# Performance work log

Hardware: AMD Instinct MI355X
Metric: run time of the kernel (lower is better)

The kernel has to match this reference:

```python
import jax, jax.numpy as jnp
import numpy as np

TOP_K = 2
SCALING = 16.0 / 8.0  # alpha / rank


def setup_inputs() -> dict:
    key = jax.random.key(0)
    ks = jax.random.split(key, 9)
    B, V, D, P = 32, 21, 512, 64
    IN, OUT, E, R, H = D * P, 96, 8, 8, 256
    return {
        "x": jax.random.normal(ks[0], (B, V, D, P), jnp.float32),
        "W_base": jax.random.normal(ks[1], (OUT, IN), jnp.float32) * (IN ** -0.5),
        "b_base": jax.random.normal(ks[2], (OUT,), jnp.float32) * 0.01,
        "W1": jax.random.normal(ks[3], (H, D), jnp.float32) * (D ** -0.5),
        "b1": jax.random.normal(ks[4], (H,), jnp.float32) * 0.01,
        "W2": jax.random.normal(ks[5], (E, H), jnp.float32) * (H ** -0.5),
        "b2": jax.random.normal(ks[6], (E,), jnp.float32) * 0.01,
        "lora_A": jax.random.normal(ks[7], (E, R, IN), jnp.float32) * (IN ** -0.5),
        "lora_B": jax.random.normal(ks[8], (E, OUT, R), jnp.float32) * (R ** -0.5),
    }


def reference(x, W_base, b_base, W1, b1, W2, b2, lora_A, lora_B):
    B, V, D, P = x.shape
    E = lora_A.shape[0]
    # FlattenHead: flatten last two dims, then linear (dropout is identity in eval)
    flat = x.reshape(B, V, D * P)                      # [B, V, IN]
    base_out = flat @ W_base.T + b_base                # [B, V, OUT]
    # Router: pool over n_vars then patch dim -> [B, D]
    pooled = x.mean(axis=1).mean(axis=-1)
    h = jax.nn.relu(pooled @ W1.T + b1)
    logits = h @ W2.T + b2                             # [B, E]
    probs = jax.nn.softmax(logits, axis=-1)
    topw, topi = jax.lax.top_k(probs, TOP_K)           # [B, K]
    topw = topw / jnp.clip(topw.sum(-1, keepdims=True), 1e-6)
    # All LoRA experts (matches original dense compute), then weighted combine
    temp = jnp.einsum("bvi,eri->ebvr", flat, lora_A)   # [E, B, V, R]
    delta = jnp.einsum("ebvr,eor->ebvo", temp, lora_B) * SCALING  # [E, B, V, OUT]
    # Scatter top-k weights into dense [B, E] then combine (top-k sparse combine)
    w_full = jnp.zeros((B, E), x.dtype).at[jnp.arange(B)[:, None], topi].add(topw)
    moe_delta = jnp.einsum("be,ebvo->bvo", w_full, delta)
    return base_out + moe_delta, probs
```

## Files before the change

kernel.cpp:

```cpp
#include <hip/hip_runtime.h>

#define B_DIM 32
#define V_DIM 21
#define D_DIM 512
#define P_DIM 64
#define M_TOTAL 672
#define K_TOTAL 32768
#define OUT_DIM 96
#define E_DIM 8
#define R_DIM 8
#define H_DIM 256
#define N_TOTAL 160
#define SCALING 2.0f
#define POOL_SCALE (1.0f / (V_DIM * (float)P_DIM))

#define BM 64
#define BK 128
#define KSPLIT 64
#define K_PER_BLOCK (K_TOTAL / KSPLIT)
#define CHUNKS (K_PER_BLOCK / BK)
#define LDS_K (BK + 8)

typedef __attribute__((ext_vector_type(4))) float floatx4;
typedef __attribute__((ext_vector_type(8))) short short8;

__device__ __forceinline__ unsigned short f2bf(float f) {
  union { float f; unsigned int u; } v; v.f = f;
  unsigned int u = v.u + (0x7FFFu + ((v.u >> 16) & 1u));
  return (unsigned short)(u >> 16);
}

__global__ __launch_bounds__(256)
void convW_kernel(const float* __restrict__ W_base, const float* __restrict__ lora_A,
                  short* __restrict__ Wb) {
  size_t base = ((size_t)blockIdx.x * 256 + threadIdx.x) * 8;
  int row = (int)(base >> 15);
  int k = (int)(base & 32767);
  const float* src = (row < OUT_DIM) ? (W_base + ((size_t)row << 15) + k)
                                     : (lora_A + ((size_t)(row - OUT_DIM) << 15) + k);
  floatx4 v0 = ((const floatx4*)src)[0];
  floatx4 v1 = ((const floatx4*)src)[1];
  short8 sv;
  sv[0] = (short)f2bf(v0[0]); sv[1] = (short)f2bf(v0[1]);
  sv[2] = (short)f2bf(v0[2]); sv[3] = (short)f2bf(v0[3]);
  sv[4] = (short)f2bf(v1[0]); sv[5] = (short)f2bf(v1[1]);
  sv[6] = (short)f2bf(v1[2]); sv[7] = (short)f2bf(v1[3]);
  *(short8*)(Wb + base) = sv;
}

__global__ __launch_bounds__(256, 2)
void gemm_kernel(const float* __restrict__ x, const short* __restrict__ Wb,
                 float* __restrict__ S, float* __restrict__ pooled) {
  __shared__ short ldsA[BM * LDS_K];
  __shared__ short ldsW[N_TOTAL * LDS_K];
  __shared__ float lds_pool[5 * 8];
  const int tid = threadIdx.x;
  const int m0 = blockIdx.x * BM;
  const int kbase = blockIdx.y * K_PER_BLOCK;
  const int lane = tid & 63;
  const int wave = tid >> 6;
  const int quad = lane >> 4;
  const int l16 = lane & 15;
  const int mhalf = (wave & 1) * 32;
  const int nhalf = (wave >> 1) * 80;
  const int b_first = m0 / V_DIM;
  const int d_first = kbase >> 6;

  if (tid < 40) lds_pool[tid] = 0.0f;

  floatx4 acc[2][5];
  #pragma unroll
  for (int mt = 0; mt < 2; ++mt)
    #pragma unroll
    for (int nt = 0; nt < 5; ++nt) acc[mt][nt] = (floatx4)(0.0f);

  const int a_row0 = tid >> 4;
  const int a_g = tid & 15;

  floatx4 pa[8];
  short8  pw[10];

#define ISSUE_LOADS(c)                                                          \
  {                                                                             \
    const int kc = kbase + (c) * BK;                                            \
    _Pragma("unroll")                                                           \
    for (int it = 0; it < 4; ++it) {                                            \
      int row = a_row0 + it * 16;                                               \
      int m = m0 + row;                                                         \
      if (m < M_TOTAL) {                                                        \
        const floatx4* s4 = (const floatx4*)(x + (size_t)m * K_TOTAL + kc + a_g * 8); \
        pa[it * 2] = s4[0];                                                     \
        pa[it * 2 + 1] = s4[1];                                                 \
      } else {                                                                  \
        pa[it * 2] = (floatx4)(0.0f);                                           \
        pa[it * 2 + 1] = (floatx4)(0.0f);                                       \
      }                                                                         \
    }                                                                           \
    _Pragma("unroll")                                                           \
    for (int it = 0; it < 10; ++it) {                                           \
      int idx = it * 256 + tid;                                                 \
      int row = idx >> 4;                                                       \
      int g = idx & 15;                                                         \
      pw[it] = *(const short8*)(Wb + (size_t)row * K_TOTAL + kc + g * 8);       \
    }                                                                           \
  }

#define CONVERT_WRITE(c)                                                        \
  {                                                                             \
    const int kc = kbase + (c) * BK;                                            \
    _Pragma("unroll")                                                           \
    for (int it = 0; it < 4; ++it) {                                            \
      int row = a_row0 + it * 16;                                               \
      int m = m0 + row;                                                         \
      floatx4 v0 = pa[it * 2], v1 = pa[it * 2 + 1];                             \
      if (m < M_TOTAL) {                                                        \
        float sum8 = ((v0[0] + v0[1]) + (v0[2] + v0[3])) +                      \
                     ((v1[0] + v1[1]) + (v1[2] + v1[3]));                       \
        int b_local = (m / V_DIM) - b_first;                                    \
        int d_local = ((kc + a_g * 8) >> 6) - d_first;                          \
        atomicAdd(&lds_pool[b_local * 8 + d_local], sum8);                      \
      }                                                                         \
      short8 sv;                                                                \
      sv[0] = (short)f2bf(v0[0]); sv[1] = (short)f2bf(v0[1]);                   \
      sv[2] = (short)f2bf(v0[2]); sv[3] = (short)f2bf(v0[3]);                   \
      sv[4] = (short)f2bf(v1[0]); sv[5] = (short)f2bf(v1[1]);                   \
      sv[6] = (short)f2bf(v1[2]); sv[7] = (short)f2bf(v1[3]);                   \
      *(short8*)&ldsA[row * LDS_K + a_g * 8] = sv;                              \
    }                                                                           \
    _Pragma("unroll")                                                           \
    for (int it = 0; it < 10; ++it) {                                           \
      int idx = it * 256 + tid;                                                 \
      int row = idx >> 4;                                                       \
      int g = idx & 15;                                                         \
      *(short8*)&ldsW[row * LDS_K + g * 8] = pw[it];                            \
    }                                                                           \
  }

  ISSUE_LOADS(0);
  __syncthreads();
  CONVERT_WRITE(0);

  for (int c = 0; c < CHUNKS; ++c) {
    __syncthreads();
    if (c + 1 < CHUNKS) ISSUE_LOADS(c + 1);
    #pragma unroll
    for (int ks = 0; ks < 4; ++ks) {
      const int ko = ks * 32 + quad * 8;
      short8 a0 = *(const short8*)&ldsA[(mhalf + l16) * LDS_K + ko];
      short8 a1 = *(const short8*)&ldsA[(mhalf + 16 + l16) * LDS_K + ko];
      #pragma unroll
      for (int nt = 0; nt < 5; ++nt) {
        short8 b = *(const short8*)&ldsW[(nhalf + nt * 16 + l16) * LDS_K + ko];
        acc[0][nt] = __builtin_amdgcn_mfma_f32_16x16x32_bf16(a0, b, acc[0][nt], 0, 0, 0);
        acc[1][nt] = __builtin_amdgcn_mfma_f32_16x16x32_bf16(a1, b, acc[1][nt], 0, 0, 0);
      }
    }
    __syncthreads();
    if (c + 1 < CHUNKS) CONVERT_WRITE(c + 1);
  }

  #pragma unroll
  for (int mt = 0; mt < 2; ++mt)
    #pragma unroll
    for (int nt = 0; nt < 5; ++nt)
      #pragma unroll
      for (int r = 0; r < 4; ++r) {
        int m = m0 + mhalf + mt * 16 + quad * 4 + r;
        int n = nhalf + nt * 16 + l16;
        if (m < M_TOTAL) atomicAdd(&S[(size_t)m * N_TOTAL + n], acc[mt][nt][r]);
      }

  if (tid < 40) {
    int b = b_first + (tid >> 3);
    int d = d_first + (tid & 7);
    if (b < B_DIM)
      atomicAdd(&pooled[b * D_DIM + d], lds_pool[tid] * POOL_SCALE);
  }
}

__global__ __launch_bounds__(256)
void router_kernel(const float* __restrict__ pooled, const float* __restrict__ W1,
                   const float* __restrict__ b1, const float* __restrict__ W2,
                   const float* __restrict__ b2, float* __restrict__ wfull,
                   float* __restrict__ probs_out) {
  __shared__ float sp[D_DIM];
  __shared__ float sh[H_DIM];
  __shared__ float slog[E_DIM];
  const int b = blockIdx.x;
  const int t = threadIdx.x;
  sp[t] = pooled[b * D_DIM + t];
  sp[t + 256] = pooled[b * D_DIM + t + 256];
  __syncthreads();
  float acc = b1[t];
  const float* w1r = W1 + (size_t)t * D_DIM;
  for (int d = 0; d < D_DIM; ++d) acc += sp[d] * w1r[d];
  sh[t] = fmaxf(acc, 0.0f);
  __syncthreads();
  if (t < E_DIM) {
    float a = b2[t];
    const float* w2r = W2 + t * H_DIM;
    for (int j = 0; j < H_DIM; ++j) a += sh[j] * w2r[j];
    slog[t] = a;
  }
  __syncthreads();
  if (t == 0) {
    float p[E_DIM];
    float mx = slog[0];
    for (int e = 1; e < E_DIM; ++e) mx = fmaxf(mx, slog[e]);
    float se = 0.0f;
    for (int e = 0; e < E_DIM; ++e) { p[e] = __expf(slog[e] - mx); se += p[e]; }
    float inv = 1.0f / se;
    for (int e = 0; e < E_DIM; ++e) { p[e] *= inv; probs_out[b * E_DIM + e] = p[e]; }
    int i0 = 0;
    for (int e = 1; e < E_DIM; ++e) if (p[e] > p[i0]) i0 = e;
    int i1 = (i0 == 0) ? 1 : 0;
    for (int e = 0; e < E_DIM; ++e) if (e != i0 && p[e] > p[i1]) i1 = e;
    float s2 = p[i0] + p[i1];
    float invs = 1.0f / fmaxf(s2, 1e-6f);
    for (int e = 0; e < E_DIM; ++e) {
      float w = 0.0f;
      if (e == i0) w += p[i0] * invs;
      if (e == i1) w += p[i1] * invs;
      wfull[b * E_DIM + e] = w;
    }
  }
}

__global__ __launch_bounds__(256)
void combine_kernel(const float* __restrict__ S, const float* __restrict__ b_base,
                    const float* __restrict__ lora_B, const float* __restrict__ wfull,
                    float* __restrict__ out) {
  int idx = blockIdx.x * 256 + threadIdx.x;
  if (idx >= M_TOTAL * OUT_DIM) return;
  int bv = idx / OUT_DIM;
  int o = idx - bv * OUT_DIM;
  int b = bv / V_DIM;
  const float* srow = S + (size_t)bv * N_TOTAL;
  float base = srow[o] + b_base[o];
  float moe = 0.0f;
  #pragma unroll
  for (int e = 0; e < E_DIM; ++e) {
    float we = wfull[b * E_DIM + e];
    if (we != 0.0f) {
      const float* lb = lora_B + ((size_t)e * OUT_DIM + o) * R_DIM;
      const float* tr = srow + OUT_DIM + e * R_DIM;
      float d = 0.0f;
      #pragma unroll
      for (int r = 0; r < R_DIM; ++r) d += tr[r] * lb[r];
      moe += we * d;
    }
  }
  out[idx] = base + SCALING * moe;
}

extern "C" void kernel_launch(void* const* d_in, const int* in_sizes, int n_in,
                              void* d_out, int out_size, void* d_ws, size_t ws_size,
                              hipStream_t stream) {
  const float* x      = (const float*)d_in[0];
  const float* W_base = (const float*)d_in[1];
  const float* b_base = (const float*)d_in[2];
  const float* W1     = (const float*)d_in[3];
  const float* b1     = (const float*)d_in[4];
  const float* W2     = (const float*)d_in[5];
  const float* b2     = (const float*)d_in[6];
  const float* lora_A = (const float*)d_in[7];
  const float* lora_B = (const float*)d_in[8];
  float* out = (float*)d_out;

  float* ws     = (float*)d_ws;
  float* pooled = ws;
  float* S      = ws + 16384;
  float* wfull  = ws + 16384 + (size_t)M_TOTAL * N_TOTAL;
  short* Wb     = (short*)(wfull + 256);

  hipMemsetAsync(d_ws, 0, (16384 + (size_t)M_TOTAL * N_TOTAL) * sizeof(float), stream);

  convW_kernel<<<(N_TOTAL * K_TOTAL / 8 + 255) / 256, 256, 0, stream>>>(W_base, lora_A, Wb);
  gemm_kernel<<<dim3(11, KSPLIT), 256, 0, stream>>>(x, Wb, S, pooled);
  router_kernel<<<B_DIM, 256, 0, stream>>>(pooled, W1, b1, W2, b2, wfull,
                                           out + (size_t)M_TOTAL * OUT_DIM);
  combine_kernel<<<(M_TOTAL * OUT_DIM + 255) / 256, 256, 0, stream>>>(
      S, b_base, lora_B, wfull, out);
}
```

Measured before the change: 217.5 us.

## Load W fragments directly from global into registers, drop W LDS staging

The GEMM kernel no longer stages the bf16 weight tile in LDS. Each wave now reads its B-operand MFMA fragments straight from global memory, and only the activation tile goes through LDS. BK is halved to 64 and the pooling partial sums are reduced with a 16-lane shuffle before the LDS atomic. Smaller LDS use allows three blocks per CU instead of two, but the uncoalesced per-lane W loads are issued without prefetch, which can expose global latency and double the number of sync rounds.

```diff
diff --git a/kernel.cpp b/kernel.cpp
--- a/kernel.cpp
+++ b/kernel.cpp
@@ -15,7 +15,7 @@
 #define POOL_SCALE (1.0f / (V_DIM * (float)P_DIM))
 
 #define BM 64
-#define BK 128
+#define BK 64
 #define KSPLIT 64
 #define K_PER_BLOCK (K_TOTAL / KSPLIT)
 #define CHUNKS (K_PER_BLOCK / BK)
@@ -23,6 +23,7 @@
 
 typedef __attribute__((ext_vector_type(4))) float floatx4;
 typedef __attribute__((ext_vector_type(8))) short short8;
+typedef __attribute__((ext_vector_type(4))) short shortx4;
 
 __device__ __forceinline__ unsigned short f2bf(float f) {
   union { float f; unsigned int u; } v; v.f = f;
@@ -48,11 +49,10 @@
   *(short8*)(Wb + base) = sv;
 }
 
-__global__ __launch_bounds__(256, 2)
+__global__ __launch_bounds__(256, 3)
 void gemm_kernel(const float* __restrict__ x, const short* __restrict__ Wb,
                  float* __restrict__ S, float* __restrict__ pooled) {
   __shared__ short ldsA[BM * LDS_K];
-  __shared__ short ldsW[N_TOTAL * LDS_K];
   __shared__ float lds_pool[5 * 8];
   const int tid = threadIdx.x;
   const int m0 = blockIdx.x * BM;
@@ -74,85 +74,73 @@
     #pragma unroll
     for (int nt = 0; nt < 5; ++nt) acc[mt][nt] = (floatx4)(0.0f);
 
-  const int a_row0 = tid >> 4;
-  const int a_g = tid & 15;
-
-  floatx4 pa[8];
-  short8  pw[10];
-
-#define ISSUE_LOADS(c)                                                          \
+  floatx4 pa[4];
+
+#define ISSUE_A(c)                                                              \
   {                                                                             \
     const int kc = kbase + (c) * BK;                                            \
     _Pragma("unroll")                                                           \
     for (int it = 0; it < 4; ++it) {                                            \
-      int row = a_row0 + it * 16;                                               \
-      int m = m0 + row;                                                         \
-      if (m < M_TOTAL) {                                                        \
-        const floatx4* s4 = (const floatx4*)(x + (size_t)m * K_TOTAL + kc + a_g * 8); \
-        pa[it * 2] = s4[0];                                                     \
-        pa[it * 2 + 1] = s4[1];                                                 \
-      } else {                                                                  \
-        pa[it * 2] = (floatx4)(0.0f);                                           \
-        pa[it * 2 + 1] = (floatx4)(0.0f);                                       \
-      }                                                                         \
-    }                                                                           \
-    _Pragma("unroll")                                                           \
-    for (int it = 0; it < 10; ++it) {                                           \
       int idx = it * 256 + tid;                                                 \
       int row = idx >> 4;                                                       \
-      int g = idx & 15;                                                         \
-      pw[it] = *(const short8*)(Wb + (size_t)row * K_TOTAL + kc + g * 8);       \
+      int u = idx & 15;                                                         \
+      int m = m0 + row;                                                         \
+      pa[it] = (m < M_TOTAL)                                                    \
+          ? *(const floatx4*)(x + (size_t)m * K_TOTAL + kc + u * 4)             \
+          : (floatx4)(0.0f);                                                    \
     }                                                                           \
   }
 
 #define CONVERT_WRITE(c)                                                        \
   {                                                                             \
-    const int kc = kbase + (c) * BK;                                            \
     _Pragma("unroll")                                                           \
     for (int it = 0; it < 4; ++it) {                                            \
-      int row = a_row0 + it * 16;                                               \
-      int m = m0 + row;                                                         \
-      floatx4 v0 = pa[it * 2], v1 = pa[it * 2 + 1];                             \
-      if (m < M_TOTAL) {                                                        \
-        float sum8 = ((v0[0] + v0[1]) + (v0[2] + v0[3])) +                      \
-                     ((v1[0] + v1[1]) + (v1[2] + v1[3]));                       \
-        int b_local = (m / V_DIM) - b_first;                                    \
-        int d_local = ((kc + a_g * 8) >> 6) - d_first;                          \
-        atomicAdd(&lds_pool[b_local * 8 + d_local], sum8);                      \
-      }                                                                         \
-      short8 sv;                                                                \
-      sv[0] = (short)f2bf(v0[0]); sv[1] = (short)f2bf(v0[1]);                   \
-      sv[2] = (short)f2bf(v0[2]); sv[3] = (short)f2bf(v0[3]);                   \
-      sv[4] = (short)f2bf(v1[0]); sv[5] = (short)f2bf(v1[1]);                   \
-      sv[6] = (short)f2bf(v1[2]); sv[7] = (short)f2bf(v1[3]);                   \
-      *(short8*)&ldsA[row * LDS_K + a_g * 8] = sv;                              \
-    }                                                                           \
-    _Pragma("unroll")                                                           \
-    for (int it = 0; it < 10; ++it) {                                           \
       int idx = it * 256 + tid;                                                 \
       int row = idx >> 4;                                                       \
-      int g = idx & 15;                                                         \
-      *(short8*)&ldsW[row * LDS_K + g * 8] = pw[it];                            \
+      int u = idx & 15;                                                         \
+      int m = m0 + row;                                                         \
+      floatx4 v = pa[it];                                                       \
+       \
+      float s4 = (v[0] + v[1]) + (v[2] + v[3]);                                 \
+      s4 += __shfl_down(s4, 8, 16);                                             \
+      s4 += __shfl_down(s4, 4, 16);                                             \
+      s4 += __shfl_down(s4, 2, 16);                                             \
+      s4 += __shfl_down(s4, 1, 16);                                             \
+      if (u == 0 && m < M_TOTAL) {                                              \
+        int b_local = (m / V_DIM) - b_first;                                    \
+        atomicAdd(&lds_pool[b_local * 8 + (c)], s4);                            \
+      }                                                                         \
+      shortx4 sv;                                                               \
+      sv[0] = (short)f2bf(v[0]); sv[1] = (short)f2bf(v[1]);                     \
+      sv[2] = (short)f2bf(v[2]); sv[3] = (short)f2bf(v[3]);                     \
+      *(shortx4*)&ldsA[row * LDS_K + u * 4] = sv;                               \
     }                                                                           \
   }
 
-  ISSUE_LOADS(0);
+  ISSUE_A(0);
   __syncthreads();
   CONVERT_WRITE(0);
 
   for (int c = 0; c < CHUNKS; ++c) {
     __syncthreads();
-    if (c + 1 < CHUNKS) ISSUE_LOADS(c + 1);
-    #pragma unroll
-    for (int ks = 0; ks < 4; ++ks) {
+    if (c + 1 < CHUNKS) ISSUE_A(c + 1);
+    const int kc = kbase + c * BK;
+    short8 bf[2][5];
+    #pragma unroll
+    for (int ks = 0; ks < 2; ++ks)
+      #pragma unroll
+      for (int nt = 0; nt < 5; ++nt)
+        bf[ks][nt] = *(const short8*)(Wb + (size_t)(nhalf + nt * 16 + l16) * K_TOTAL
+                                      + kc + ks * 32 + quad * 8);
+    #pragma unroll
+    for (int ks = 0; ks < 2; ++ks) {
       const int ko = ks * 32 + quad * 8;
       short8 a0 = *(const short8*)&ldsA[(mhalf + l16) * LDS_K + ko];
       short8 a1 = *(const short8*)&ldsA[(mhalf + 16 + l16) * LDS_K + ko];
       #pragma unroll
       for (int nt = 0; nt < 5; ++nt) {
-        short8 b = *(const short8*)&ldsW[(nhalf + nt * 16 + l16) * LDS_K + ko];
-        acc[0][nt] = __builtin_amdgcn_mfma_f32_16x16x32_bf16(a0, b, acc[0][nt], 0, 0, 0);
-        acc[1][nt] = __builtin_amdgcn_mfma_f32_16x16x32_bf16(a1, b, acc[1][nt], 0, 0, 0);
+        acc[0][nt] = __builtin_amdgcn_mfma_f32_16x16x32_bf16(a0, bf[ks][nt], acc[0][nt], 0, 0, 0);
+        acc[1][nt] = __builtin_amdgcn_mfma_f32_16x16x32_bf16(a1, bf[ks][nt], acc[1][nt], 0, 0, 0);
       }
     }
     __syncthreads();
@@ -273,7 +261,7 @@
   float* wfull  = ws + 16384 + (size_t)M_TOTAL * N_TOTAL;
   short* Wb     = (short*)(wfull + 256);
 
-  hipMemsetAsync(d_ws, 0, (16384 + (size_t)M_TOTAL * N_TOTAL) * sizeof(float), stream);
+  (void)hipMemsetAsync(d_ws, 0, (16384 + (size_t)M_TOTAL * N_TOTAL) * sizeof(float), stream);
 
   convW_kernel<<<(N_TOTAL * K_TOTAL / 8 + 255) / 256, 256, 0, stream>>>(W_base, lora_A, Wb);
   gemm_kernel<<<dim3(11, KSPLIT), 256, 0, stream>>>(x, Wb, S, pooled);
```

New measurement: 227.2 us. 4.5% more time.
